# Optimization experiments

Hardware: AMD Instinct MI355X
Metric: run time of the kernel (lower is better)

Reference implementation:

```python
import jax, jax.numpy as jnp
import numpy as np

N_HEADS = 16
HIDDEN = 256
DIM = 4096
SEQ_LEN = 4096
BATCH = 8192
DECAY_CONSTANT = SEQ_LEN // 512  # = 8


def setup_inputs() -> dict:
    key = jax.random.key(0)
    ks = jax.random.split(key, 9)
    return {
        "x": jax.random.normal(ks[0], (BATCH, DIM), dtype=jnp.float32),
        "proj_w": jax.random.normal(ks[1], (N_HEADS, HIDDEN, DIM), dtype=jnp.float32) * 0.02,
        "proj_b": jax.random.normal(ks[2], (N_HEADS, HIDDEN), dtype=jnp.float32) * 0.02,
        "mix_w": jax.random.normal(ks[3], (N_HEADS, SEQ_LEN), dtype=jnp.float32) * 0.02 + 1.0,
        "mix_b": jax.random.normal(ks[4], (N_HEADS, SEQ_LEN), dtype=jnp.float32) * 0.02,
        "decay_value": jax.random.uniform(ks[5], (N_HEADS,), dtype=jnp.float32, minval=0.85, maxval=1.05),
        "cache": jax.random.normal(ks[6], (N_HEADS, BATCH, HIDDEN), dtype=jnp.float32),
        "out_w": jax.random.normal(ks[7], (DIM, DIM), dtype=jnp.float32) * 0.02,
        "out_b": jax.random.normal(ks[8], (DIM,), dtype=jnp.float32) * 0.02,
        "index": 1000,
    }


def reference(x, proj_w, proj_b, mix_w, mix_b, decay_value, cache, out_w, out_b, index):
    # Per-head projections: [h, b, k]
    proj = jnp.einsum("bd,hkd->hbk", x, proj_w) + proj_b[:, None, :]

    # Mixer params at the given sequence index (scalar per head)
    w = mix_w[:, index]          # [h]
    b = mix_b[:, index]          # [h]
    decay = jnp.clip(decay_value, 0.9, 1.0) ** (1.0 / DECAY_CONSTANT)  # [h]

    # First n_heads//2 heads are Col-style: out = w*x + w*decay*cache + b
    # Last  n_heads//2 heads are Row-style: out = w*x +   decay*cache + b
    is_col = jnp.arange(N_HEADS) < (N_HEADS // 2)
    cache_coef = jnp.where(is_col, w * decay, decay)  # [h]

    out = (w[:, None, None] * proj
           + cache_coef[:, None, None] * cache
           + b[:, None, None])  # [h, b, k]

    # Concatenate heads along feature axis -> [batch, n_heads*hidden] = [batch, dim]
    hidden = jnp.transpose(out, (1, 0, 2)).reshape(x.shape[0], N_HEADS * HIDDEN)

    return hidden @ out_w.T + out_b
```

## Files before the change

### kernel.cpp

```cpp
#include <hip/hip_runtime.h>
#include <hip/hip_bf16.h>

#define MROW 8192
#define DIMK 4096
#define NCOL 4096
#define HID  256
#define NH   16
#define SEQL 4096

#define BKT 32
#define NKT (DIMK / BKT)
#define SLOTB 32768
#define LDS_TOTAL (4 * SLOTB)

typedef __attribute__((ext_vector_type(8))) short short8;
typedef __attribute__((ext_vector_type(4))) float f32x4;

#define SBAR() asm volatile("s_barrier" ::: "memory")

__device__ inline ushort f2bf(float f) {
  unsigned u = __float_as_uint(f);
  u += 0x7FFF + ((u >> 16) & 1);
  return (ushort)(u >> 16);
}

__device__ inline void gload16(const void* g, void* l) {
  __builtin_amdgcn_global_load_lds(
      (const __attribute__((address_space(1))) void*)g,
      (__attribute__((address_space(3))) void*)l, 16, 0, 0);
}

__global__ void cvt_f32_bf16(const float* __restrict__ s, ushort* __restrict__ d, long n8) {
  long stride = (long)gridDim.x * blockDim.x;
  for (long i = (long)blockIdx.x * blockDim.x + threadIdx.x; i < n8; i += stride) {
    const float4* s4 = (const float4*)(s + i * 8);
    float4 a = s4[0], b = s4[1];
    ushort r[8] = {f2bf(a.x), f2bf(a.y), f2bf(a.z), f2bf(a.w),
                   f2bf(b.x), f2bf(b.y), f2bf(b.z), f2bf(b.w)};
    *(uint4*)(d + i * 8) = *(const uint4*)r;
  }
}

__global__ void coef_kernel(const float* __restrict__ mix_w, const float* __restrict__ mix_b,
                            const float* __restrict__ decay_value, const float* __restrict__ proj_b,
                            const int* __restrict__ index_p,
                            float* __restrict__ wv, float* __restrict__ cc, float* __restrict__ pb2) {
  int n = blockIdx.x * blockDim.x + threadIdx.x;
  if (n >= NCOL) return;
  int h = n >> 8;
  int idx = *index_p;
  float w  = mix_w[h * SEQL + idx];
  float bb = mix_b[h * SEQL + idx];
  float dv = fminf(fmaxf(decay_value[h], 0.9f), 1.0f);
  float decay = powf(dv, 0.125f);
  float coef = (h < NH / 2) ? w * decay : decay;
  wv[n]  = w;
  cc[n]  = coef;
  pb2[n] = w * proj_b[n] + bb;
}

template <int EPI>
__global__ __launch_bounds__(1024, 4) void gemm256(
    const ushort* __restrict__ A, const ushort* __restrict__ B,
    float* __restrict__ outf, ushort* __restrict__ outh,
    const float* __restrict__ cache, const float* __restrict__ wv,
    const float* __restrict__ cc, const float* __restrict__ pb2,
    const float* __restrict__ outb) {
  extern __shared__ __align__(16) char smem[];

  const int tid  = threadIdx.x;
  const int lane = tid & 63;
  const int wid  = tid >> 6;
  const int wr = wid >> 2;
  const int wc = wid & 3;
  const int r16 = lane & 15;
  const int cq  = lane >> 4;

  const int bid = blockIdx.x;
  const int swz = (bid & 7) * 64 + (bid >> 3);
  const int bm = swz >> 4, bn = swz & 15;
  const int m0 = bm * 256, n0 = bn * 256;

  const ushort* Ag = A + (size_t)m0 * DIMK;
  const ushort* Bg = B + (size_t)n0 * DIMK;

  int aoff[4], boff[4];
#pragma unroll
  for (int i = 0; i < 4; ++i) {
    int arow = wr * 64 + i * 16 + r16;
    aoff[i] = arow * 64 + ((cq ^ ((arow >> 1) & 3)) << 4);
    int brow = wc * 64 + i * 16 + r16;
    boff[i] = 16384 + brow * 64 + ((cq ^ ((brow >> 1) & 3)) << 4);
  }

  const int soff = tid * 16;
  const int srow = soff >> 6;
  const int sgo  = srow * DIMK + ((((soff >> 4) & 3) ^ ((srow >> 1) & 3)) << 3);

  f32x4 acc[4][4] = {};

#pragma unroll
  for (int kt = 0; kt < 3; ++kt) {
    char* s = smem + kt * SLOTB;
    gload16(Ag + (size_t)sgo + kt * BKT, s + soff);
    gload16(Bg + (size_t)sgo + kt * BKT, s + 16384 + soff);
  }
  asm volatile("s_waitcnt vmcnt(4)" ::: "memory");
  SBAR();

  for (int kt = 0; kt < NKT; ++kt) {
    const char* cur = smem + (kt & 3) * SLOTB;

    short8 af[4], bf[4];
#pragma unroll
    for (int i = 0; i < 4; ++i) bf[i] = *(const short8*)(cur + boff[i]);
#pragma unroll
    for (int i = 0; i < 4; ++i) af[i] = *(const short8*)(cur + aoff[i]);

    if (kt < NKT - 3) {
      char* st = smem + ((kt + 3) & 3) * SLOTB;
      int k0 = (kt + 3) * BKT;
      gload16(Ag + (size_t)sgo + k0, st + soff);
      gload16(Bg + (size_t)sgo + k0, st + 16384 + soff);
    }

    __builtin_amdgcn_s_setprio(1);
#pragma unroll
    for (int mi = 0; mi < 4; ++mi)
#pragma unroll
      for (int ni = 0; ni < 4; ++ni)
        acc[mi][ni] = __builtin_amdgcn_mfma_f32_16x16x32_bf16(af[mi], bf[ni], acc[mi][ni], 0, 0, 0);
    __builtin_amdgcn_s_setprio(0);

    if (kt < NKT - 3)       asm volatile("s_waitcnt vmcnt(4)" ::: "memory");
    else if (kt == NKT - 3) asm volatile("s_waitcnt vmcnt(2)" ::: "memory");
    else if (kt == NKT - 2) asm volatile("s_waitcnt vmcnt(0)" ::: "memory");
    SBAR();
  }

  const int colb = n0 + wc * 64 + r16;
  const int rowb = m0 + wr * 64 + cq * 4;

  float wvv[4], ccv[4], pbv[4], obv[4];
#pragma unroll
  for (int ni = 0; ni < 4; ++ni) {
    int n = colb + ni * 16;
    if (EPI == 1) { wvv[ni] = wv[n]; ccv[ni] = cc[n]; pbv[ni] = pb2[n]; }
    else          { obv[ni] = outb[n]; }
  }

#pragma unroll
  for (int mi = 0; mi < 4; ++mi) {
#pragma unroll
    for (int ni = 0; ni < 4; ++ni) {
      f32x4 v = acc[mi][ni];
      int n = colb + ni * 16;
#pragma unroll
      for (int r = 0; r < 4; ++r) {
        int m = rowb + mi * 16 + r;
        if (EPI == 1) {
          int h = n >> 8, kq = n & 255;
          float val = wvv[ni] * v[r] + ccv[ni] * cache[((size_t)h * MROW + m) * HID + kq] + pbv[ni];
          outh[(size_t)m * NCOL + n] = f2bf(val);
        } else {
          outf[(size_t)m * NCOL + n] = v[r] + obv[ni];
        }
      }
    }
  }
}

extern "C" void kernel_launch(void* const* d_in, const int* in_sizes, int n_in,
                              void* d_out, int out_size, void* d_ws, size_t ws_size,
                              hipStream_t stream) {
  const float* x      = (const float*)d_in[0];
  const float* proj_w = (const float*)d_in[1];
  const float* proj_b = (const float*)d_in[2];
  const float* mix_w  = (const float*)d_in[3];
  const float* mix_b  = (const float*)d_in[4];
  const float* decay  = (const float*)d_in[5];
  const float* cache  = (const float*)d_in[6];
  const float* out_w  = (const float*)d_in[7];
  const float* out_b  = (const float*)d_in[8];
  const int*   index  = (const int*)d_in[9];

  char* ws = (char*)d_ws;
  ushort* xb  = (ushort*)ws;
  ushort* pwb = (ushort*)(ws + 67108864);
  ushort* owb = (ushort*)(ws + 100663296);
  ushort* hid = (ushort*)(ws + 134217728);
  float*  wv  = (float*)(ws + 201326592);
  float*  cc  = (float*)(ws + 201326592 + 16384);
  float*  pb2 = (float*)(ws + 201326592 + 32768);

  hipFuncSetAttribute((const void*)&gemm256<1>, hipFuncAttributeMaxDynamicSharedMemorySize, LDS_TOTAL);
  hipFuncSetAttribute((const void*)&gemm256<0>, hipFuncAttributeMaxDynamicSharedMemorySize, LDS_TOTAL);

  hipLaunchKernelGGL(cvt_f32_bf16, dim3(2048), dim3(256), 0, stream,
                     x, xb, (long)MROW * DIMK / 8);
  hipLaunchKernelGGL(cvt_f32_bf16, dim3(1024), dim3(256), 0, stream,
                     proj_w, pwb, (long)NCOL * DIMK / 8);
  hipLaunchKernelGGL(cvt_f32_bf16, dim3(1024), dim3(256), 0, stream,
                     out_w, owb, (long)NCOL * DIMK / 8);
  hipLaunchKernelGGL(coef_kernel, dim3(16), dim3(256), 0, stream,
                     mix_w, mix_b, decay, proj_b, index, wv, cc, pb2);

  hipLaunchKernelGGL((gemm256<1>), dim3((MROW / 256) * (NCOL / 256)), dim3(1024), LDS_TOTAL, stream,
                     xb, pwb, nullptr, hid, cache, wv, cc, pb2, nullptr);
  hipLaunchKernelGGL((gemm256<0>), dim3((MROW / 256) * (NCOL / 256)), dim3(1024), LDS_TOTAL, stream,
                     hid, owb, (float*)d_out, nullptr, nullptr, nullptr, nullptr, nullptr, out_b);
}
```

Baseline: 597.7 us.

## Use K=64 tiles with double buffering and 128x64 per-wave GEMM tiles

Rewrites the GEMM main loop to load 64-wide K slices into two 64KB LDS slots instead of four 32KB slots, using 512-thread blocks where each wave computes a 128x64 output sub-tile. The LDS swizzle is changed to an XOR over 8 16-byte chunks per 128-byte row. The goal is to halve the number of barriers per K and increase register-level operand reuse per MFMA. In exchange, prefetch depth drops to a single tile ahead with a full vmcnt(0) wait each iteration, and accumulator register pressure doubles.

New measurement: 587.1 us. Within noise of the previous version (-1.8%).

```diff
diff --git a/kernel.cpp b/kernel.cpp
--- a/kernel.cpp
+++ b/kernel.cpp
@@ -8,10 +8,10 @@
 #define NH   16
 #define SEQL 4096
 
-#define BKT 32
+#define BKT 64
 #define NKT (DIMK / BKT)
-#define SLOTB 32768
-#define LDS_TOTAL (4 * SLOTB)
+#define SLOTB 65536
+#define LDS_TOTAL (2 * SLOTB)
 
 typedef __attribute__((ext_vector_type(8))) short short8;
 typedef __attribute__((ext_vector_type(4))) float f32x4;
@@ -60,7 +60,7 @@
 }
 
 template <int EPI>
-__global__ __launch_bounds__(1024, 4) void gemm256(
+__global__ __launch_bounds__(512, 2) void gemmk64(
     const ushort* __restrict__ A, const ushort* __restrict__ B,
     float* __restrict__ outf, ushort* __restrict__ outh,
     const float* __restrict__ cache, const float* __restrict__ wv,
@@ -84,62 +84,77 @@
   const ushort* Ag = A + (size_t)m0 * DIMK;
   const ushort* Bg = B + (size_t)n0 * DIMK;
 
-  int aoff[4], boff[4];
-#pragma unroll
-  for (int i = 0; i < 4; ++i) {
-    int arow = wr * 64 + i * 16 + r16;
-    aoff[i] = arow * 64 + ((cq ^ ((arow >> 1) & 3)) << 4);
-    int brow = wc * 64 + i * 16 + r16;
-    boff[i] = 16384 + brow * 64 + ((cq ^ ((brow >> 1) & 3)) << 4);
-  }
-
-  const int soff = tid * 16;
-  const int srow = soff >> 6;
-  const int sgo  = srow * DIMK + ((((soff >> 4) & 3) ^ ((srow >> 1) & 3)) << 3);
-
-  f32x4 acc[4][4] = {};
-
-#pragma unroll
-  for (int kt = 0; kt < 3; ++kt) {
-    char* s = smem + kt * SLOTB;
-    gload16(Ag + (size_t)sgo + kt * BKT, s + soff);
-    gload16(Bg + (size_t)sgo + kt * BKT, s + 16384 + soff);
-  }
-  asm volatile("s_waitcnt vmcnt(4)" ::: "memory");
+  const int ax0 = ((0 * 4 + cq) ^ (r16 & 7)) << 4;
+  const int ax1 = ((1 * 4 + cq) ^ (r16 & 7)) << 4;
+  const int abase = (wr * 128 + r16) * 128;
+  const int bbase = 32768 + (wc * 64 + r16) * 128;
+
+  const int srow = tid >> 3;
+  const int sgo  = srow * DIMK + (((tid & 7) ^ (srow & 7)) << 3);
+  const int ldst = tid * 16;
+
+  f32x4 acc[8][4] = {};
+
+#pragma unroll
+  for (int g = 0; g < 4; ++g) {
+    gload16(Ag + (size_t)sgo + (size_t)g * 64 * DIMK, smem + ldst + g * 8192);
+    gload16(Bg + (size_t)sgo + (size_t)g * 64 * DIMK, smem + 32768 + ldst + g * 8192);
+  }
+  asm volatile("s_waitcnt vmcnt(0)" ::: "memory");
   SBAR();
+  __builtin_amdgcn_sched_barrier(0);
 
   for (int kt = 0; kt < NKT; ++kt) {
-    const char* cur = smem + (kt & 3) * SLOTB;
-
-    short8 af[4], bf[4];
-#pragma unroll
-    for (int i = 0; i < 4; ++i) bf[i] = *(const short8*)(cur + boff[i]);
-#pragma unroll
-    for (int i = 0; i < 4; ++i) af[i] = *(const short8*)(cur + aoff[i]);
-
-    if (kt < NKT - 3) {
-      char* st = smem + ((kt + 3) & 3) * SLOTB;
-      int k0 = (kt + 3) * BKT;
-      gload16(Ag + (size_t)sgo + k0, st + soff);
-      gload16(Bg + (size_t)sgo + k0, st + 16384 + soff);
-    }
-
-    __builtin_amdgcn_s_setprio(1);
-#pragma unroll
-    for (int mi = 0; mi < 4; ++mi)
-#pragma unroll
-      for (int ni = 0; ni < 4; ++ni)
-        acc[mi][ni] = __builtin_amdgcn_mfma_f32_16x16x32_bf16(af[mi], bf[ni], acc[mi][ni], 0, 0, 0);
-    __builtin_amdgcn_s_setprio(0);
-
-    if (kt < NKT - 3)       asm volatile("s_waitcnt vmcnt(4)" ::: "memory");
-    else if (kt == NKT - 3) asm volatile("s_waitcnt vmcnt(2)" ::: "memory");
-    else if (kt == NKT - 2) asm volatile("s_waitcnt vmcnt(0)" ::: "memory");
+    const char* cur = smem + (kt & 1) * SLOTB;
+    const bool  do_st = kt + 1 < NKT;
+
+    if (do_st) {
+      char* st = smem + ((kt + 1) & 1) * SLOTB;
+      const size_t k0 = (size_t)(kt + 1) * BKT;
+#pragma unroll
+      for (int g = 0; g < 4; ++g) {
+        gload16(Ag + (size_t)sgo + (size_t)g * 64 * DIMK + k0, st + ldst + g * 8192);
+        gload16(Bg + (size_t)sgo + (size_t)g * 64 * DIMK + k0, st + 32768 + ldst + g * 8192);
+      }
+    }
+
+    {
+      short8 af[8], bf[4];
+#pragma unroll
+      for (int i = 0; i < 8; ++i) af[i] = *(const short8*)(cur + abase + ax0 + i * 2048);
+#pragma unroll
+      for (int i = 0; i < 4; ++i) bf[i] = *(const short8*)(cur + bbase + ax0 + i * 2048);
+      __builtin_amdgcn_s_setprio(1);
+#pragma unroll
+      for (int mi = 0; mi < 8; ++mi)
+#pragma unroll
+        for (int ni = 0; ni < 4; ++ni)
+          acc[mi][ni] = __builtin_amdgcn_mfma_f32_16x16x32_bf16(af[mi], bf[ni], acc[mi][ni], 0, 0, 0);
+      __builtin_amdgcn_s_setprio(0);
+    }
+    {
+      short8 af[8], bf[4];
+#pragma unroll
+      for (int i = 0; i < 8; ++i) af[i] = *(const short8*)(cur + abase + ax1 + i * 2048);
+#pragma unroll
+      for (int i = 0; i < 4; ++i) bf[i] = *(const short8*)(cur + bbase + ax1 + i * 2048);
+      __builtin_amdgcn_s_setprio(1);
+#pragma unroll
+      for (int mi = 0; mi < 8; ++mi)
+#pragma unroll
+        for (int ni = 0; ni < 4; ++ni)
+          acc[mi][ni] = __builtin_amdgcn_mfma_f32_16x16x32_bf16(af[mi], bf[ni], acc[mi][ni], 0, 0, 0);
+      __builtin_amdgcn_s_setprio(0);
+    }
+
+    if (do_st) asm volatile("s_waitcnt vmcnt(0)" ::: "memory");
+    asm volatile("s_waitcnt lgkmcnt(0)" ::: "memory");
     SBAR();
+    __builtin_amdgcn_sched_barrier(0);
   }
 
   const int colb = n0 + wc * 64 + r16;
-  const int rowb = m0 + wr * 64 + cq * 4;
+  const int rowb = m0 + wr * 128 + cq * 4;
 
   float wvv[4], ccv[4], pbv[4], obv[4];
 #pragma unroll
@@ -150,14 +165,15 @@
   }
 
 #pragma unroll
-  for (int mi = 0; mi < 4; ++mi) {
+  for (int am = 0; am < 8; ++am) {
+    int mrow = rowb + am * 16;
 #pragma unroll
     for (int ni = 0; ni < 4; ++ni) {
-      f32x4 v = acc[mi][ni];
+      f32x4 v = acc[am][ni];
       int n = colb + ni * 16;
 #pragma unroll
       for (int r = 0; r < 4; ++r) {
-        int m = rowb + mi * 16 + r;
+        int m = mrow + r;
         if (EPI == 1) {
           int h = n >> 8, kq = n & 255;
           float val = wvv[ni] * v[r] + ccv[ni] * cache[((size_t)h * MROW + m) * HID + kq] + pbv[ni];
@@ -193,8 +209,8 @@
   float*  cc  = (float*)(ws + 201326592 + 16384);
   float*  pb2 = (float*)(ws + 201326592 + 32768);
 
-  hipFuncSetAttribute((const void*)&gemm256<1>, hipFuncAttributeMaxDynamicSharedMemorySize, LDS_TOTAL);
-  hipFuncSetAttribute((const void*)&gemm256<0>, hipFuncAttributeMaxDynamicSharedMemorySize, LDS_TOTAL);
+  hipFuncSetAttribute((const void*)&gemmk64<1>, hipFuncAttributeMaxDynamicSharedMemorySize, LDS_TOTAL);
+  hipFuncSetAttribute((const void*)&gemmk64<0>, hipFuncAttributeMaxDynamicSharedMemorySize, LDS_TOTAL);
 
   hipLaunchKernelGGL(cvt_f32_bf16, dim3(2048), dim3(256), 0, stream,
                      x, xb, (long)MROW * DIMK / 8);
@@ -205,8 +221,8 @@
   hipLaunchKernelGGL(coef_kernel, dim3(16), dim3(256), 0, stream,
                      mix_w, mix_b, decay, proj_b, index, wv, cc, pb2);
 
-  hipLaunchKernelGGL((gemm256<1>), dim3((MROW / 256) * (NCOL / 256)), dim3(1024), LDS_TOTAL, stream,
+  hipLaunchKernelGGL((gemmk64<1>), dim3((MROW / 256) * (NCOL / 256)), dim3(512), LDS_TOTAL, stream,
                      xb, pwb, nullptr, hid, cache, wv, cc, pb2, nullptr);
-  hipLaunchKernelGGL((gemm256<0>), dim3((MROW / 256) * (NCOL / 256)), dim3(1024), LDS_TOTAL, stream,
+  hipLaunchKernelGGL((gemmk64<0>), dim3((MROW / 256) * (NCOL / 256)), dim3(512), LDS_TOTAL, stream,
                      hid, owb, (float*)d_out, nullptr, nullptr, nullptr, nullptr, nullptr, out_b);
 }
```
